# Performance work log

Hardware: AMD Instinct MI355X
Metric: run time of the kernel (lower is better)

## Reference

```python
import jax, jax.numpy as jnp
import numpy as np

B, T, N, D, R, K, P = 4, 336, 862, 64, 8, 6, 96


def setup_inputs() -> dict:
    key = jax.random.key(0)
    ks = jax.random.split(key, 8)
    s = 0.02
    return {
        "x_enc": jax.random.normal(ks[0], (B, T, N), jnp.float32),
        "W_embed": jax.random.normal(ks[1], (1, D), jnp.float32) * s,
        "b_embed": jnp.zeros((D,), jnp.float32),
        "W1": jax.random.normal(ks[2], (D, R), jnp.float32) * s,
        "W2": jax.random.normal(ks[3], (D, R), jnp.float32) * s,
        "gate": jnp.float32(-4.0),  # gate_init
        "A_prior": jnp.eye(N, dtype=jnp.float32),  # season_gcn_adj_source=identity
        "W_gcn": jax.random.normal(ks[4], (D, D), jnp.float32) * s,
        "g_gcn": jnp.float32(0.5),  # season_gcn gate
        "W_head": jax.random.normal(ks[5], (T * D, P), jnp.float32) * s,
        "b_head": jnp.zeros((P,), jnp.float32),
    }


def _topk_renorm(adj, k):
    # keep top-k entries per row, zero the rest, renormalize rows (matches _sparsify_adj)
    vals = jax.lax.top_k(adj, k)[0]
    thresh = vals[..., -1:]
    mask = (adj >= thresh).astype(adj.dtype)
    masked = adj * mask
    denom = jnp.clip(jnp.sum(masked, axis=-1, keepdims=True), 1e-12, None)
    return masked / denom


def reference(x_enc, W_embed, b_embed, W1, W2, gate, A_prior, W_gcn, g_gcn, W_head, b_head):
    # per-variable, per-timestep value embedding: [B,N,T,D]
    h = x_enc.transpose(0, 2, 1)[..., None] * W_embed[0] + b_embed
    # content-mean node descriptors: [B,N,D]
    z = jnp.mean(h, axis=2)
    # low-rank graph learner -> adjacency logits [B,N,N]
    e1 = z @ W1
    e2 = z @ W2
    logits = jnp.einsum('bnr,bmr->bnm', e1, e2) / jnp.sqrt(jnp.float32(R))
    adj = jax.nn.softmax(logits, axis=-1)
    adj = _topk_renorm(adj, K)  # top-k sparsify + row renorm
    # gated graph mixing over variable nodes
    h_mix = jnp.einsum('bnm,bmtd->bntd', adj, h)
    h = h + jax.nn.sigmoid(gate) * h_mix
    # season GCN: sym-normalized prior adjacency, residual + gate
    deg = jnp.sum(A_prior, axis=-1)
    dinv = jnp.where(deg > 0, 1.0 / jnp.sqrt(deg), 0.0)
    A_hat = A_prior * dinv[:, None] * dinv[None, :]
    h = h + g_gcn * jnp.einsum('nm,bmtd,de->bnte', A_hat, h, W_gcn)
    # forecast head: flatten tokens, project to pred_len per variable
    out = h.reshape(B, N, T * D) @ W_head + b_head  # [B,N,P]
    return out.transpose(0, 2, 1)  # [B,P,N]
```

## Files before the change

### kernel.cpp

```cpp
#include <hip/hip_runtime.h>
#include <math.h>

#define B_ 4
#define T_ 336
#define N_ 862
#define D_ 64
#define R_ 8
#define K_ 6
#define P_ 96
#define NR 896
#define CAP 32
#define NB 864

#define OFF_PCQ  0
#define OFF_XBP  768
#define OFF_DINV 21504
#define OFF_WGT  22368
#define OFF_IDX  43104
#define OFF_CNT  63840
#define OFF_CSRV 64704
#define OFF_CSRI 92352
#define OFF_P12  120000
#define OFF_PCP  184512
#define OFF_XPT  249024

__global__ __launch_bounds__(192) void kA_prep(const float* __restrict__ x,
                                               const float* __restrict__ Whead,
                                               const float* __restrict__ A,
                                               const float* __restrict__ We,
                                               const float* __restrict__ be,
                                               const float* __restrict__ gate,
                                               const float* __restrict__ Wgcn,
                                               float* __restrict__ ws) {
  int id = blockIdx.x;
  int tid = threadIdx.x;
  if (id < 336) {
    __shared__ float sW1[64], sW2[64], sCB[64], sWe[64];
    int t = id;
    float g = 1.f / (1.f + expf(-gate[0]));
    if (tid < 64) {
      float a = 0.f;
#pragma unroll
      for (int dd = 0; dd < D_; ++dd) a += We[dd] * Wgcn[dd * D_ + tid];
      sW1[tid] = a;
    } else if (tid < 128) {
      int e = tid - 64;
      float a = 0.f;
#pragma unroll
      for (int dd = 0; dd < D_; ++dd) a += be[dd] * Wgcn[dd * D_ + e];
      sW2[e] = (1.f + g) * a;
    } else {
      int e = tid - 128;
      sCB[e] = (1.f + g) * be[e];
      sWe[e] = We[e];
    }
    __syncthreads();
    int c = tid, p = c % P_, sel = c / P_;
    const float* cA = sel ? sW1 : sWe;
    const float* cB = sel ? sW2 : sCB;
    const float* wrow = Whead + (size_t)t * D_ * P_ + p;
    float a = 0.f, bacc = 0.f;
#pragma unroll
    for (int e = 0; e < D_; ++e) {
      float w = wrow[(size_t)e * P_];
      a = fmaf(cA[e], w, a);
      bacc = fmaf(cB[e], w, bacc);
    }
    ws[OFF_P12 + t * 192 + c] = a;
    ws[OFF_PCP + t * 192 + c] = bacc;
  } else if (id < 672) {
    __shared__ float part[192];
    int iq = id - 336;
    int b = iq / 84, rem = iq % 84;
    int ch = rem / 6, tg = rem % 6;
    int lane = tid & 63, tsub = tid >> 6;
    int n = ch * 64 + lane;
    float s = 0.f;
    if (n < N_) {
      const float* xp = x + (size_t)(b * T_) * N_ + n;
      int tend = tg * 56 + 56;
#pragma unroll 4
      for (int t = tg * 56 + tsub; t < tend; t += 3) s += xp[(size_t)t * N_];
    }
    part[tid] = s;
    __syncthreads();
    if (tsub == 0 && n < N_)
      ws[OFF_XBP + (size_t)(b * 6 + tg) * NB + n] =
          part[lane] + part[64 + lane] + part[128 + lane];
  } else {
    int lane = tid & 63, wv = tid >> 6;
    int n = (id - 672) * 3 + wv;
    if (n >= N_) return;
    const float* ap = A + (size_t)n * N_;
    float* vout = ws + OFF_CSRV;
    int* iout = (int*)(ws + OFF_CSRI);
    float s = 0.f;
    int total = 0;
    for (int base = 0; base < N_; base += 64) {
      int m = base + lane;
      float a = (m < N_) ? ap[m] : 0.f;
      s += a;
      bool nz = (a != 0.f);
      unsigned long long mask = __ballot(nz);
      int pos = __popcll(mask & ((1ull << lane) - 1ull));
      if (nz) {
        int slot = total + pos;
        if (slot < CAP) { vout[slot * NB + n] = a; iout[slot * NB + n] = m; }
      }
      total += __popcll(mask);
    }
    for (int off = 32; off; off >>= 1) s += __shfl_down(s, off);
    if (lane == 0) {
      ws[OFF_DINV + n] = (s > 0.f) ? (1.f / sqrtf(s)) : 0.f;
      ((int*)(ws + OFF_CNT))[n] = (total <= CAP) ? total : -1;
    }
  }
}

__global__ __launch_bounds__(192) void kM_mid(const float* __restrict__ x,
                                              const float* __restrict__ W1,
                                              const float* __restrict__ W2,
                                              const float* __restrict__ We,
                                              const float* __restrict__ be,
                                              const float* __restrict__ gate,
                                              float* __restrict__ ws) {
  __shared__ float smem[5376];
  int id = blockIdx.x;
  int tid = threadIdx.x;
  if (id < 432) {
    float* xs = smem;
    float* ps = smem + 768;
    int b = id / 108;
    int rem = id % 108;
    int n0 = (rem >> 1) * 16;
    int ch = (rem & 1) * 96;
    int cq = tid % 24, nq = tid / 24;
    int c0 = cq * 4;
    const float* P = ws + OFF_P12;
    float acc[4][2];
#pragma unroll
    for (int i = 0; i < 4; ++i) { acc[i][0] = 0.f; acc[i][1] = 0.f; }
    int xrow = tid >> 2, xcol4 = tid & 3;
    for (int kc = 0; kc < 7; ++kc) {
      int t0 = kc * 48;
      {
        const float* xr = x + (size_t)(b * T_ + t0 + xrow) * N_;
        if (n0 + 15 < N_) {
          *(float4*)(xs + xrow * 16 + xcol4 * 4) = *(const float4*)(xr + n0 + xcol4 * 4);
        } else {
          float* dst = xs + xrow * 16 + xcol4 * 4;
#pragma unroll
          for (int q = 0; q < 4; ++q) {
            int nn = n0 + xcol4 * 4 + q; if (nn > N_ - 1) nn = N_ - 1;
            dst[q] = xr[nn];
          }
        }
      }
#pragma unroll
      for (int sIdx = 0; sIdx < 6; ++sIdx) {
        int i4 = tid + sIdx * 192;
        int row = i4 / 24, col4 = i4 % 24;
        *(float4*)(ps + row * 96 + col4 * 4) =
            *(const float4*)(P + (size_t)(t0 + row) * 192 + ch + col4 * 4);
      }
      __syncthreads();
#pragma unroll 6
      for (int kk = 0; kk < 48; ++kk) {
        float x0 = xs[kk * 16 + nq * 2];
        float x1 = xs[kk * 16 + nq * 2 + 1];
        float4 pv = *(const float4*)(ps + kk * 96 + c0);
        acc[0][0] = fmaf(pv.x, x0, acc[0][0]); acc[0][1] = fmaf(pv.x, x1, acc[0][1]);
        acc[1][0] = fmaf(pv.y, x0, acc[1][0]); acc[1][1] = fmaf(pv.y, x1, acc[1][1]);
        acc[2][0] = fmaf(pv.z, x0, acc[2][0]); acc[2][1] = fmaf(pv.z, x1, acc[2][1]);
        acc[3][0] = fmaf(pv.w, x0, acc[3][0]); acc[3][1] = fmaf(pv.w, x1, acc[3][1]);
      }
      __syncthreads();
    }
    int n = n0 + nq * 2;
#pragma unroll
    for (int cc = 0; cc < 4; ++cc) {
      float* op = ws + OFF_XPT + ((size_t)(b * 192 + ch + c0 + cc)) * NR + n;
      if (n + 1 < N_) { float2 v; v.x = acc[cc][0]; v.y = acc[cc][1]; *(float2*)op = v; }
      else if (n < N_) { op[0] = acc[cc][0]; }
    }
  } else if (id < 436) {
    __shared__ float s_sc[4][R_];
    __shared__ float s_scal[5];
    __shared__ float selv[12];
    __shared__ int seli[12];
    float* sx = smem;
    float* wkmax = smem + 864;
    float* wkmin = smem + 1728;
    int b = id - 432;
    if (tid < 16) {
      int r = tid & 7, which = tid >> 3;
      const float* W = which ? W2 : W1;
      float a = 0.f, bb = 0.f;
      for (int dd = 0; dd < D_; ++dd) {
        float w = W[dd * R_ + r];
        a += We[dd] * w; bb += be[dd] * w;
      }
      s_sc[which * 2][r] = a; s_sc[which * 2 + 1][r] = bb;
    }
    const float invT = 1.f / (float)T_;
    for (int i = tid; i < NB; i += 192) {
      float v = 0.f;
      if (i < N_) {
        const float* xp = ws + OFF_XBP + (size_t)(b * 6) * NB + i;
#pragma unroll
        for (int q = 0; q < 6; ++q) v += xp[q * NB];
        v *= invT;
      }
      sx[i] = v;
      wkmax[i] = (i < N_) ? v : -3.4e38f;
      wkmin[i] = (i < N_) ? v : 3.4e38f;
    }
    __syncthreads();
    if (tid == 0) {
      float s11 = 0.f, s12 = 0.f, s21 = 0.f, s22 = 0.f;
      for (int r = 0; r < R_; ++r) {
        s11 += s_sc[0][r] * s_sc[2][r];
        s12 += s_sc[0][r] * s_sc[3][r];
        s21 += s_sc[1][r] * s_sc[2][r];
        s22 += s_sc[1][r] * s_sc[3][r];
      }
      s_scal[0] = s11; s_scal[1] = s12; s_scal[2] = s21; s_scal[3] = s22;
      s_scal[4] = 1.f / (1.f + expf(-gate[0]));
    }
    if (tid < 64) {
      int lane = tid;
      for (int r = 0; r < K_; ++r) {
        float bv = -3.4e38f; int bi = 0;
        for (int i = lane; i < N_; i += 64) {
          float v = wkmax[i];
          if (v > bv) { bv = v; bi = i; }
        }
        for (int off = 32; off; off >>= 1) {
          float ov = __shfl_down(bv, off);
          int oi = __shfl_down(bi, off);
          if (ov > bv) { bv = ov; bi = oi; }
        }
        bv = __shfl(bv, 0); bi = __shfl(bi, 0);
        if (lane == 0) { selv[r] = bv; seli[r] = bi; wkmax[bi] = -3.4e38f; }
      }
    } else if (tid < 128) {
      int lane = tid - 64;
      for (int r = 0; r < K_; ++r) {
        float bv = 3.4e38f; int bi = 0;
        for (int i = lane; i < N_; i += 64) {
          float v = wkmin[i];
          if (v < bv) { bv = v; bi = i; }
        }
        for (int off = 32; off; off >>= 1) {
          float ov = __shfl_down(bv, off);
          int oi = __shfl_down(bi, off);
          if (ov < bv) { bv = ov; bi = oi; }
        }
        bv = __shfl(bv, 0); bi = __shfl(bi, 0);
        if (lane == 0) { selv[6 + r] = bv; seli[6 + r] = bi; wkmin[bi] = 3.4e38f; }
      }
    }
    __syncthreads();
    float s11 = s_scal[0], s12 = s_scal[1], s21 = s_scal[2], s22 = s_scal[3];
    float g = s_scal[4];
    const float rsq = 0.3535533906f;
    for (int n = tid; n < N_; n += 192) {
      float xn = sx[n];
      float alpha = (xn * s11 + s21) * rsq;
      float beta  = (xn * s12 + s22) * rsq;
      int base = (alpha >= 0.f) ? 0 : 6;
      float l[K_]; float mx = -3.4e38f;
#pragma unroll
      for (int j = 0; j < K_; ++j) { l[j] = alpha * selv[base + j] + beta; mx = fmaxf(mx, l[j]); }
      float e[K_]; float ss = 0.f;
#pragma unroll
      for (int j = 0; j < K_; ++j) { e[j] = expf(l[j] - mx); ss += e[j]; }
      float sc = g / ss;
#pragma unroll
      for (int j = 0; j < K_; ++j) {
        ws[OFF_WGT + j * (4 * NB) + b * NB + n] = e[j] * sc;
        ((int*)(ws + OFF_IDX))[j * (4 * NB) + b * NB + n] = seli[base + j];
      }
    }
  } else {
    int q = id - 436;
    if (tid < 192) {
      float s = 0.f;
#pragma unroll 12
      for (int t = q * 84; t < q * 84 + 84; ++t) s += ws[OFF_PCP + t * 192 + tid];
      ws[OFF_PCQ + q * 192 + tid] = s;
    }
  }
}

__global__ __launch_bounds__(256) void kF_final(const float* __restrict__ A,
                                                const float* __restrict__ bhead,
                                                const float* __restrict__ ggcn,
                                                const float* __restrict__ ws,
                                                float* __restrict__ out) {
  int c = blockIdx.y;
  int n = blockIdx.x * 256 + threadIdx.x;
  if (n >= N_) return;
  int b = c / P_, p = c % P_;
  const float* Xp1 = ws + OFF_XPT + ((size_t)(b * 192 + p)) * NR;
  const float* Xp2 = ws + OFF_XPT + ((size_t)(b * 192 + P_ + p)) * NR;
  const float* WGTb = ws + OFF_WGT + b * NB;
  const int* IDXb = (const int*)(ws + OFF_IDX) + b * NB;
  float gg = ggcn[0];
  float PCp = 0.f, PAp = 0.f;
#pragma unroll
  for (int q = 0; q < 4; ++q) {
    PCp += ws[OFF_PCQ + q * 192 + p];
    PAp += ws[OFF_PCQ + q * 192 + 96 + p];
  }
  float wj[K_]; int ij[K_];
#pragma unroll
  for (int j = 0; j < K_; ++j) {
    wj[j] = WGTb[j * (4 * NB) + n];
    ij[j] = IDXb[j * (4 * NB) + n];
  }
  float acc1 = Xp1[n];
#pragma unroll
  for (int j = 0; j < K_; ++j) acc1 += wj[j] * Xp1[ij[j]];
  int cnt = ((const int*)(ws + OFF_CNT))[n];
  float S = 0.f;
  if (cnt >= 0) {
    const float* vv = ws + OFF_CSRV;
    const int* ii = (const int*)(ws + OFF_CSRI);
    for (int jj = 0; jj < cnt; ++jj) {
      float a = vv[jj * NB + n];
      int m = ii[jj * NB + n];
      float mix2 = Xp2[m];
      if (m == n) {
#pragma unroll
        for (int j = 0; j < K_; ++j) mix2 += wj[j] * Xp2[ij[j]];
      } else {
#pragma unroll
        for (int j = 0; j < K_; ++j)
          mix2 += WGTb[j * (4 * NB) + m] * Xp2[IDXb[j * (4 * NB) + m]];
      }
      S += a * ws[OFF_DINV + m] * (mix2 + PAp);
    }
  } else {
    const float* ar = A + (size_t)n * N_;
    for (int m = 0; m < N_; ++m) {
      float a = ar[m];
      if (a != 0.f) {
        float mix2 = Xp2[m];
#pragma unroll
        for (int j = 0; j < K_; ++j)
          mix2 += WGTb[j * (4 * NB) + m] * Xp2[IDXb[j * (4 * NB) + m]];
        S += a * ws[OFF_DINV + m] * (mix2 + PAp);
      }
    }
  }
  out[(size_t)c * N_ + n] = acc1 + gg * ws[OFF_DINV + n] * S + PCp + bhead[p];
}

extern "C" void kernel_launch(void* const* d_in, const int* in_sizes, int n_in,
                              void* d_out, int out_size, void* d_ws, size_t ws_size,
                              hipStream_t stream) {
  const float* x     = (const float*)d_in[0];
  const float* We    = (const float*)d_in[1];
  const float* be    = (const float*)d_in[2];
  const float* W1    = (const float*)d_in[3];
  const float* W2    = (const float*)d_in[4];
  const float* gate  = (const float*)d_in[5];
  const float* A     = (const float*)d_in[6];
  const float* Wgcn  = (const float*)d_in[7];
  const float* ggcn  = (const float*)d_in[8];
  const float* Whead = (const float*)d_in[9];
  const float* bhead = (const float*)d_in[10];
  float* ws = (float*)d_ws;
  float* out = (float*)d_out;

  kA_prep<<<960, 192, 0, stream>>>(x, Whead, A, We, be, gate, Wgcn, ws);
  kM_mid<<<440, 192, 0, stream>>>(x, W1, W2, We, be, gate, ws);
  kF_final<<<dim3(4, 384), 256, 0, stream>>>(A, bhead, ggcn, ws, out);
}
```

Baseline: 110.2 us.

## Fuse three kernels into one persistent kernel with atomic grid barriers

Merges the prep, mid and final kernels into a single persistent kernel of 512 blocks that loops over virtual block indices and separates the stages with software grid barriers built on atomic counters. A memset before the launch clears the barrier counters. The goal is to remove the launch gaps and tail drain between kernels. In exchange it adds barrier spin costs, leaves threads idle in stages written for 192 threads, adds a memset call, and relies on all 512 blocks being co-resident to avoid deadlock.

```diff
diff --git a/kernel.cpp b/kernel.cpp
--- a/kernel.cpp
+++ b/kernel.cpp
@@ -23,338 +23,360 @@
 #define OFF_P12  120000
 #define OFF_PCP  184512
 #define OFF_XPT  249024
-
-__global__ __launch_bounds__(192) void kA_prep(const float* __restrict__ x,
-                                               const float* __restrict__ Whead,
-                                               const float* __restrict__ A,
-                                               const float* __restrict__ We,
-                                               const float* __restrict__ be,
-                                               const float* __restrict__ gate,
-                                               const float* __restrict__ Wgcn,
-                                               float* __restrict__ ws) {
-  int id = blockIdx.x;
+#define OFF_BAR  937216
+
+#define GRID_ 512
+
+__device__ __forceinline__ void grid_barrier(int* ctr) {
+  __threadfence();
+  __syncthreads();
+  if (threadIdx.x == 0) {
+    __hip_atomic_fetch_add(ctr, 1, __ATOMIC_ACQ_REL, __HIP_MEMORY_SCOPE_AGENT);
+    while (__hip_atomic_load(ctr, __ATOMIC_ACQUIRE, __HIP_MEMORY_SCOPE_AGENT) < GRID_) {
+      __builtin_amdgcn_s_sleep(2);
+    }
+  }
+  __syncthreads();
+  __threadfence();
+}
+
+__global__ __launch_bounds__(256, 2) void kFused(
+    const float* __restrict__ x,    const float* __restrict__ We,
+    const float* __restrict__ be,   const float* __restrict__ W1,
+    const float* __restrict__ W2,   const float* __restrict__ gate,
+    const float* __restrict__ A,    const float* __restrict__ Wgcn,
+    const float* __restrict__ ggcn, const float* __restrict__ Whead,
+    const float* __restrict__ bhead, float* __restrict__ ws,
+    float* __restrict__ out) {
+  __shared__ float smem[5376];
   int tid = threadIdx.x;
-  if (id < 336) {
-    __shared__ float sW1[64], sW2[64], sCB[64], sWe[64];
-    int t = id;
-    float g = 1.f / (1.f + expf(-gate[0]));
-    if (tid < 64) {
-      float a = 0.f;
-#pragma unroll
-      for (int dd = 0; dd < D_; ++dd) a += We[dd] * Wgcn[dd * D_ + tid];
-      sW1[tid] = a;
-    } else if (tid < 128) {
-      int e = tid - 64;
-      float a = 0.f;
-#pragma unroll
-      for (int dd = 0; dd < D_; ++dd) a += be[dd] * Wgcn[dd * D_ + e];
-      sW2[e] = (1.f + g) * a;
+
+  for (int vb = blockIdx.x; vb < 888; vb += GRID_) {
+    __syncthreads();
+    if (vb < 336) {
+      float* sW1 = smem;
+      float* sW2 = smem + 64;
+      float* sCB = smem + 128;
+      float* sWe = smem + 192;
+      int t = vb;
+      float g = 1.f / (1.f + expf(-gate[0]));
+      if (tid < 64) {
+        float a = 0.f;
+#pragma unroll
+        for (int dd = 0; dd < D_; ++dd) a += We[dd] * Wgcn[dd * D_ + tid];
+        sW1[tid] = a;
+      } else if (tid < 128) {
+        int e = tid - 64;
+        float a = 0.f;
+#pragma unroll
+        for (int dd = 0; dd < D_; ++dd) a += be[dd] * Wgcn[dd * D_ + e];
+        sW2[e] = (1.f + g) * a;
+      } else if (tid < 192) {
+        int e = tid - 128;
+        sCB[e] = (1.f + g) * be[e];
+        sWe[e] = We[e];
+      }
+      __syncthreads();
+      if (tid < 192) {
+        int c = tid, p = c % P_, sel = c / P_;
+        const float* cA = sel ? sW1 : sWe;
+        const float* cB = sel ? sW2 : sCB;
+        const float* wrow = Whead + (size_t)t * D_ * P_ + p;
+        float a = 0.f, bacc = 0.f;
+#pragma unroll
+        for (int e = 0; e < D_; ++e) {
+          float w = wrow[(size_t)e * P_];
+          a = fmaf(cA[e], w, a);
+          bacc = fmaf(cB[e], w, bacc);
+        }
+        ws[OFF_P12 + t * 192 + c] = a;
+        ws[OFF_PCP + t * 192 + c] = bacc;
+      }
+    } else if (vb < 672) {
+      float* part = smem;
+      int iq = vb - 336;
+      int b = iq / 84, rem = iq % 84;
+      int ch = rem / 6, tg = rem % 6;
+      int lane = tid & 63, tsub = tid >> 6;
+      int n = ch * 64 + lane;
+      float s = 0.f;
+      if (n < N_) {
+        const float* xp = x + (size_t)(b * T_) * N_ + n;
+        int tend = tg * 56 + 56;
+#pragma unroll 4
+        for (int t = tg * 56 + tsub; t < tend; t += 4) s += xp[(size_t)t * N_];
+      }
+      part[tid] = s;
+      __syncthreads();
+      if (tsub == 0 && n < N_)
+        ws[OFF_XBP + (size_t)(b * 6 + tg) * NB + n] =
+            part[lane] + part[64 + lane] + part[128 + lane] + part[192 + lane];
     } else {
-      int e = tid - 128;
-      sCB[e] = (1.f + g) * be[e];
-      sWe[e] = We[e];
-    }
+      int lane = tid & 63, wv = tid >> 6;
+      int n = (vb - 672) * 4 + wv;
+      if (n < N_) {
+        const float* ap = A + (size_t)n * N_;
+        float* vout = ws + OFF_CSRV;
+        int* iout = (int*)(ws + OFF_CSRI);
+        float s = 0.f;
+        int total = 0;
+        for (int base = 0; base < N_; base += 64) {
+          int m = base + lane;
+          float a = (m < N_) ? ap[m] : 0.f;
+          s += a;
+          bool nz = (a != 0.f);
+          unsigned long long mask = __ballot(nz);
+          int pos = __popcll(mask & ((1ull << lane) - 1ull));
+          if (nz) {
+            int slot = total + pos;
+            if (slot < CAP) { vout[slot * NB + n] = a; iout[slot * NB + n] = m; }
+          }
+          total += __popcll(mask);
+        }
+        for (int off = 32; off; off >>= 1) s += __shfl_down(s, off);
+        if (lane == 0) {
+          ws[OFF_DINV + n] = (s > 0.f) ? (1.f / sqrtf(s)) : 0.f;
+          ((int*)(ws + OFF_CNT))[n] = (total <= CAP) ? total : -1;
+        }
+      }
+    }
+  }
+
+  grid_barrier((int*)(ws + OFF_BAR));
+
+  for (int vb = blockIdx.x; vb < 440; vb += GRID_) {
     __syncthreads();
-    int c = tid, p = c % P_, sel = c / P_;
-    const float* cA = sel ? sW1 : sWe;
-    const float* cB = sel ? sW2 : sCB;
-    const float* wrow = Whead + (size_t)t * D_ * P_ + p;
-    float a = 0.f, bacc = 0.f;
-#pragma unroll
-    for (int e = 0; e < D_; ++e) {
-      float w = wrow[(size_t)e * P_];
-      a = fmaf(cA[e], w, a);
-      bacc = fmaf(cB[e], w, bacc);
-    }
-    ws[OFF_P12 + t * 192 + c] = a;
-    ws[OFF_PCP + t * 192 + c] = bacc;
-  } else if (id < 672) {
-    __shared__ float part[192];
-    int iq = id - 336;
-    int b = iq / 84, rem = iq % 84;
-    int ch = rem / 6, tg = rem % 6;
-    int lane = tid & 63, tsub = tid >> 6;
-    int n = ch * 64 + lane;
-    float s = 0.f;
-    if (n < N_) {
-      const float* xp = x + (size_t)(b * T_) * N_ + n;
-      int tend = tg * 56 + 56;
-#pragma unroll 4
-      for (int t = tg * 56 + tsub; t < tend; t += 3) s += xp[(size_t)t * N_];
-    }
-    part[tid] = s;
-    __syncthreads();
-    if (tsub == 0 && n < N_)
-      ws[OFF_XBP + (size_t)(b * 6 + tg) * NB + n] =
-          part[lane] + part[64 + lane] + part[128 + lane];
-  } else {
-    int lane = tid & 63, wv = tid >> 6;
-    int n = (id - 672) * 3 + wv;
-    if (n >= N_) return;
-    const float* ap = A + (size_t)n * N_;
-    float* vout = ws + OFF_CSRV;
-    int* iout = (int*)(ws + OFF_CSRI);
-    float s = 0.f;
-    int total = 0;
-    for (int base = 0; base < N_; base += 64) {
-      int m = base + lane;
-      float a = (m < N_) ? ap[m] : 0.f;
-      s += a;
-      bool nz = (a != 0.f);
-      unsigned long long mask = __ballot(nz);
-      int pos = __popcll(mask & ((1ull << lane) - 1ull));
-      if (nz) {
-        int slot = total + pos;
-        if (slot < CAP) { vout[slot * NB + n] = a; iout[slot * NB + n] = m; }
-      }
-      total += __popcll(mask);
-    }
-    for (int off = 32; off; off >>= 1) s += __shfl_down(s, off);
-    if (lane == 0) {
-      ws[OFF_DINV + n] = (s > 0.f) ? (1.f / sqrtf(s)) : 0.f;
-      ((int*)(ws + OFF_CNT))[n] = (total <= CAP) ? total : -1;
+    if (vb < 432) {
+      float* xs = smem;
+      float* ps = smem + 768;
+      int b = vb / 108;
+      int rem = vb % 108;
+      int n0 = (rem >> 1) * 16;
+      int ch = (rem & 1) * 96;
+      int cq = tid % 24, nq = tid / 24;
+      int c0 = cq * 4;
+      const float* Pm = ws + OFF_P12;
+      float acc[4][2];
+#pragma unroll
+      for (int i = 0; i < 4; ++i) { acc[i][0] = 0.f; acc[i][1] = 0.f; }
+      int xrow = tid >> 2, xcol4 = tid & 3;
+      for (int kc = 0; kc < 7; ++kc) {
+        int t0 = kc * 48;
+        if (tid < 192) {
+          const float* xr = x + (size_t)(b * T_ + t0 + xrow) * N_;
+          if (n0 + 15 < N_) {
+            *(float4*)(xs + xrow * 16 + xcol4 * 4) = *(const float4*)(xr + n0 + xcol4 * 4);
+          } else {
+            float* dst = xs + xrow * 16 + xcol4 * 4;
+#pragma unroll
+            for (int q = 0; q < 4; ++q) {
+              int nn = n0 + xcol4 * 4 + q; if (nn > N_ - 1) nn = N_ - 1;
+              dst[q] = xr[nn];
+            }
+          }
+#pragma unroll
+          for (int sIdx = 0; sIdx < 6; ++sIdx) {
+            int i4 = tid + sIdx * 192;
+            int row = i4 / 24, col4 = i4 % 24;
+            *(float4*)(ps + row * 96 + col4 * 4) =
+                *(const float4*)(Pm + (size_t)(t0 + row) * 192 + ch + col4 * 4);
+          }
+        }
+        __syncthreads();
+        if (tid < 192) {
+#pragma unroll 6
+          for (int kk = 0; kk < 48; ++kk) {
+            float x0 = xs[kk * 16 + nq * 2];
+            float x1 = xs[kk * 16 + nq * 2 + 1];
+            float4 pv = *(const float4*)(ps + kk * 96 + c0);
+            acc[0][0] = fmaf(pv.x, x0, acc[0][0]); acc[0][1] = fmaf(pv.x, x1, acc[0][1]);
+            acc[1][0] = fmaf(pv.y, x0, acc[1][0]); acc[1][1] = fmaf(pv.y, x1, acc[1][1]);
+            acc[2][0] = fmaf(pv.z, x0, acc[2][0]); acc[2][1] = fmaf(pv.z, x1, acc[2][1]);
+            acc[3][0] = fmaf(pv.w, x0, acc[3][0]); acc[3][1] = fmaf(pv.w, x1, acc[3][1]);
+          }
+        }
+        __syncthreads();
+      }
+      if (tid < 192) {
+        int n = n0 + nq * 2;
+#pragma unroll
+        for (int cc = 0; cc < 4; ++cc) {
+          float* op = ws + OFF_XPT + ((size_t)(b * 192 + ch + c0 + cc)) * NR + n;
+          if (n + 1 < N_) { float2 v; v.x = acc[cc][0]; v.y = acc[cc][1]; *(float2*)op = v; }
+          else if (n < N_) { op[0] = acc[cc][0]; }
+        }
+      }
+    } else if (vb < 436) {
+      float* sx    = smem;
+      float* wkmax = smem + 864;
+      float* wkmin = smem + 1728;
+      float* s_sc  = smem + 2592;
+      float* s_scal = smem + 2624;
+      float* selv  = smem + 2629;
+      int*   seli  = (int*)(smem + 2641);
+      int b = vb - 432;
+      if (tid < 16) {
+        int r = tid & 7, which = tid >> 3;
+        const float* W = which ? W2 : W1;
+        float a = 0.f, bb = 0.f;
+        for (int dd = 0; dd < D_; ++dd) {
+          float w = W[dd * R_ + r];
+          a += We[dd] * w; bb += be[dd] * w;
+        }
+        s_sc[(which * 2) * 8 + r] = a; s_sc[(which * 2 + 1) * 8 + r] = bb;
+      }
+      const float invT = 1.f / (float)T_;
+      for (int i = tid; i < NB; i += 256) {
+        float v = 0.f;
+        if (i < N_) {
+          const float* xp = ws + OFF_XBP + (size_t)(b * 6) * NB + i;
+#pragma unroll
+          for (int q = 0; q < 6; ++q) v += xp[q * NB];
+          v *= invT;
+        }
+        sx[i] = v;
+        wkmax[i] = (i < N_) ? v : -3.4e38f;
+        wkmin[i] = (i < N_) ? v : 3.4e38f;
+      }
+      __syncthreads();
+      if (tid == 0) {
+        float s11 = 0.f, s12 = 0.f, s21 = 0.f, s22 = 0.f;
+        for (int r = 0; r < R_; ++r) {
+          s11 += s_sc[0 * 8 + r] * s_sc[2 * 8 + r];
+          s12 += s_sc[0 * 8 + r] * s_sc[3 * 8 + r];
+          s21 += s_sc[1 * 8 + r] * s_sc[2 * 8 + r];
+          s22 += s_sc[1 * 8 + r] * s_sc[3 * 8 + r];
+        }
+        s_scal[0] = s11; s_scal[1] = s12; s_scal[2] = s21; s_scal[3] = s22;
+        s_scal[4] = 1.f / (1.f + expf(-gate[0]));
+      }
+      if (tid < 64) {
+        int lane = tid;
+        for (int r = 0; r < K_; ++r) {
+          float bv = -3.4e38f; int bi = 0;
+          for (int i = lane; i < N_; i += 64) {
+            float v = wkmax[i];
+            if (v > bv) { bv = v; bi = i; }
+          }
+          for (int off = 32; off; off >>= 1) {
+            float ov = __shfl_down(bv, off);
+            int oi = __shfl_down(bi, off);
+            if (ov > bv) { bv = ov; bi = oi; }
+          }
+          bv = __shfl(bv, 0); bi = __shfl(bi, 0);
+          if (lane == 0) { selv[r] = bv; seli[r] = bi; wkmax[bi] = -3.4e38f; }
+        }
+      } else if (tid < 128) {
+        int lane = tid - 64;
+        for (int r = 0; r < K_; ++r) {
+          float bv = 3.4e38f; int bi = 0;
+          for (int i = lane; i < N_; i += 64) {
+            float v = wkmin[i];
+            if (v < bv) { bv = v; bi = i; }
+          }
+          for (int off = 32; off; off >>= 1) {
+            float ov = __shfl_down(bv, off);
+            int oi = __shfl_down(bi, off);
+            if (ov < bv) { bv = ov; bi = oi; }
+          }
+          bv = __shfl(bv, 0); bi = __shfl(bi, 0);
+          if (lane == 0) { selv[6 + r] = bv; seli[6 + r] = bi; wkmin[bi] = 3.4e38f; }
+        }
+      }
+      __syncthreads();
+      float s11 = s_scal[0], s12 = s_scal[1], s21 = s_scal[2], s22 = s_scal[3];
+      float g = s_scal[4];
+      const float rsq = 0.3535533906f;
+      for (int n = tid; n < N_; n += 256) {
+        float xn = sx[n];
+        float alpha = (xn * s11 + s21) * rsq;
+        float beta  = (xn * s12 + s22) * rsq;
+        int base = (alpha >= 0.f) ? 0 : 6;
+        float l[K_]; float mx = -3.4e38f;
+#pragma unroll
+        for (int j = 0; j < K_; ++j) { l[j] = alpha * selv[base + j] + beta; mx = fmaxf(mx, l[j]); }
+        float e[K_]; float ss = 0.f;
+#pragma unroll
+        for (int j = 0; j < K_; ++j) { e[j] = expf(l[j] - mx); ss += e[j]; }
+        float sc = g / ss;
+#pragma unroll
+        for (int j = 0; j < K_; ++j) {
+          ws[OFF_WGT + j * (4 * NB) + b * NB + n] = e[j] * sc;
+          ((int*)(ws + OFF_IDX))[j * (4 * NB) + b * NB + n] = seli[base + j];
+        }
+      }
+    } else {
+      int q = vb - 436;
+      if (tid < 192) {
+        float s = 0.f;
+#pragma unroll 12
+        for (int t = q * 84; t < q * 84 + 84; ++t) s += ws[OFF_PCP + t * 192 + tid];
+        ws[OFF_PCQ + q * 192 + tid] = s;
+      }
     }
   }
-}
-
-__global__ __launch_bounds__(192) void kM_mid(const float* __restrict__ x,
-                                              const float* __restrict__ W1,
-                                              const float* __restrict__ W2,
-                                              const float* __restrict__ We,
-                                              const float* __restrict__ be,
-                                              const float* __restrict__ gate,
-                                              float* __restrict__ ws) {
-  __shared__ float smem[5376];
-  int id = blockIdx.x;
-  int tid = threadIdx.x;
-  if (id < 432) {
-    float* xs = smem;
-    float* ps = smem + 768;
-    int b = id / 108;
-    int rem = id % 108;
-    int n0 = (rem >> 1) * 16;
-    int ch = (rem & 1) * 96;
-    int cq = tid % 24, nq = tid / 24;
-    int c0 = cq * 4;
-    const float* P = ws + OFF_P12;
-    float acc[4][2];
-#pragma unroll
-    for (int i = 0; i < 4; ++i) { acc[i][0] = 0.f; acc[i][1] = 0.f; }
-    int xrow = tid >> 2, xcol4 = tid & 3;
-    for (int kc = 0; kc < 7; ++kc) {
-      int t0 = kc * 48;
-      {
-        const float* xr = x + (size_t)(b * T_ + t0 + xrow) * N_;
-        if (n0 + 15 < N_) {
-          *(float4*)(xs + xrow * 16 + xcol4 * 4) = *(const float4*)(xr + n0 + xcol4 * 4);
+
+  grid_barrier((int*)(ws + OFF_BAR) + 8);
+
+  for (int vb = blockIdx.x; vb < 1536; vb += GRID_) {
+    int c = vb >> 2;
+    int n = (vb & 3) * 256 + tid;
+    if (n >= N_) continue;
+    int b = c / P_, p = c % P_;
+    const float* Xp1 = ws + OFF_XPT + ((size_t)(b * 192 + p)) * NR;
+    const float* Xp2 = ws + OFF_XPT + ((size_t)(b * 192 + P_ + p)) * NR;
+    const float* WGTb = ws + OFF_WGT + b * NB;
+    const int* IDXb = (const int*)(ws + OFF_IDX) + b * NB;
+    float gg = ggcn[0];
+    float PCp = 0.f, PAp = 0.f;
+#pragma unroll
+    for (int q = 0; q < 4; ++q) {
+      PCp += ws[OFF_PCQ + q * 192 + p];
+      PAp += ws[OFF_PCQ + q * 192 + 96 + p];
+    }
+    float wj[K_]; int ij[K_];
+#pragma unroll
+    for (int j = 0; j < K_; ++j) {
+      wj[j] = WGTb[j * (4 * NB) + n];
+      ij[j] = IDXb[j * (4 * NB) + n];
+    }
+    float acc1 = Xp1[n];
+#pragma unroll
+    for (int j = 0; j < K_; ++j) acc1 += wj[j] * Xp1[ij[j]];
+    int cnt = ((const int*)(ws + OFF_CNT))[n];
+    float S = 0.f;
+    if (cnt >= 0) {
+      const float* vv = ws + OFF_CSRV;
+      const int* ii = (const int*)(ws + OFF_CSRI);
+      for (int jj = 0; jj < cnt; ++jj) {
+        float a = vv[jj * NB + n];
+        int m = ii[jj * NB + n];
+        float mix2 = Xp2[m];
+        if (m == n) {
+#pragma unroll
+          for (int j = 0; j < K_; ++j) mix2 += wj[j] * Xp2[ij[j]];
         } else {
-          float* dst = xs + xrow * 16 + xcol4 * 4;
-#pragma unroll
-          for (int q = 0; q < 4; ++q) {
-            int nn = n0 + xcol4 * 4 + q; if (nn > N_ - 1) nn = N_ - 1;
-            dst[q] = xr[nn];
-          }
-        }
-      }
-#pragma unroll
-      for (int sIdx = 0; sIdx < 6; ++sIdx) {
-        int i4 = tid + sIdx * 192;
-        int row = i4 / 24, col4 = i4 % 24;
-        *(float4*)(ps + row * 96 + col4 * 4) =
-            *(const float4*)(P + (size_t)(t0 + row) * 192 + ch + col4 * 4);
-      }
-      __syncthreads();
-#pragma unroll 6
-      for (int kk = 0; kk < 48; ++kk) {
-        float x0 = xs[kk * 16 + nq * 2];
-        float x1 = xs[kk * 16 + nq * 2 + 1];
-        float4 pv = *(const float4*)(ps + kk * 96 + c0);
-        acc[0][0] = fmaf(pv.x, x0, acc[0][0]); acc[0][1] = fmaf(pv.x, x1, acc[0][1]);
-        acc[1][0] = fmaf(pv.y, x0, acc[1][0]); acc[1][1] = fmaf(pv.y, x1, acc[1][1]);
-        acc[2][0] = fmaf(pv.z, x0, acc[2][0]); acc[2][1] = fmaf(pv.z, x1, acc[2][1]);
-        acc[3][0] = fmaf(pv.w, x0, acc[3][0]); acc[3][1] = fmaf(pv.w, x1, acc[3][1]);
-      }
-      __syncthreads();
-    }
-    int n = n0 + nq * 2;
-#pragma unroll
-    for (int cc = 0; cc < 4; ++cc) {
-      float* op = ws + OFF_XPT + ((size_t)(b * 192 + ch + c0 + cc)) * NR + n;
-      if (n + 1 < N_) { float2 v; v.x = acc[cc][0]; v.y = acc[cc][1]; *(float2*)op = v; }
-      else if (n < N_) { op[0] = acc[cc][0]; }
-    }
-  } else if (id < 436) {
-    __shared__ float s_sc[4][R_];
-    __shared__ float s_scal[5];
-    __shared__ float selv[12];
-    __shared__ int seli[12];
-    float* sx = smem;
-    float* wkmax = smem + 864;
-    float* wkmin = smem + 1728;
-    int b = id - 432;
-    if (tid < 16) {
-      int r = tid & 7, which = tid >> 3;
-      const float* W = which ? W2 : W1;
-      float a = 0.f, bb = 0.f;
-      for (int dd = 0; dd < D_; ++dd) {
-        float w = W[dd * R_ + r];
-        a += We[dd] * w; bb += be[dd] * w;
-      }
-      s_sc[which * 2][r] = a; s_sc[which * 2 + 1][r] = bb;
-    }
-    const float invT = 1.f / (float)T_;
-    for (int i = tid; i < NB; i += 192) {
-      float v = 0.f;
-      if (i < N_) {
-        const float* xp = ws + OFF_XBP + (size_t)(b * 6) * NB + i;
-#pragma unroll
-        for (int q = 0; q < 6; ++q) v += xp[q * NB];
-        v *= invT;
-      }
-      sx[i] = v;
-      wkmax[i] = (i < N_) ? v : -3.4e38f;
-      wkmin[i] = (i < N_) ? v : 3.4e38f;
-    }
-    __syncthreads();
-    if (tid == 0) {
-      float s11 = 0.f, s12 = 0.f, s21 = 0.f, s22 = 0.f;
-      for (int r = 0; r < R_; ++r) {
-        s11 += s_sc[0][r] * s_sc[2][r];
-        s12 += s_sc[0][r] * s_sc[3][r];
-        s21 += s_sc[1][r] * s_sc[2][r];
-        s22 += s_sc[1][r] * s_sc[3][r];
-      }
-      s_scal[0] = s11; s_scal[1] = s12; s_scal[2] = s21; s_scal[3] = s22;
-      s_scal[4] = 1.f / (1.f + expf(-gate[0]));
-    }
-    if (tid < 64) {
-      int lane = tid;
-      for (int r = 0; r < K_; ++r) {
-        float bv = -3.4e38f; int bi = 0;
-        for (int i = lane; i < N_; i += 64) {
-          float v = wkmax[i];
-          if (v > bv) { bv = v; bi = i; }
-        }
-        for (int off = 32; off; off >>= 1) {
-          float ov = __shfl_down(bv, off);
-          int oi = __shfl_down(bi, off);
-          if (ov > bv) { bv = ov; bi = oi; }
-        }
-        bv = __shfl(bv, 0); bi = __shfl(bi, 0);
-        if (lane == 0) { selv[r] = bv; seli[r] = bi; wkmax[bi] = -3.4e38f; }
-      }
-    } else if (tid < 128) {
-      int lane = tid - 64;
-      for (int r = 0; r < K_; ++r) {
-        float bv = 3.4e38f; int bi = 0;
-        for (int i = lane; i < N_; i += 64) {
-          float v = wkmin[i];
-          if (v < bv) { bv = v; bi = i; }
-        }
-        for (int off = 32; off; off >>= 1) {
-          float ov = __shfl_down(bv, off);
-          int oi = __shfl_down(bi, off);
-          if (ov < bv) { bv = ov; bi = oi; }
-        }
-        bv = __shfl(bv, 0); bi = __shfl(bi, 0);
-        if (lane == 0) { selv[6 + r] = bv; seli[6 + r] = bi; wkmin[bi] = 3.4e38f; }
-      }
-    }
-    __syncthreads();
-    float s11 = s_scal[0], s12 = s_scal[1], s21 = s_scal[2], s22 = s_scal[3];
-    float g = s_scal[4];
-    const float rsq = 0.3535533906f;
-    for (int n = tid; n < N_; n += 192) {
-      float xn = sx[n];
-      float alpha = (xn * s11 + s21) * rsq;
-      float beta  = (xn * s12 + s22) * rsq;
-      int base = (alpha >= 0.f) ? 0 : 6;
-      float l[K_]; float mx = -3.4e38f;
-#pragma unroll
-      for (int j = 0; j < K_; ++j) { l[j] = alpha * selv[base + j] + beta; mx = fmaxf(mx, l[j]); }
-      float e[K_]; float ss = 0.f;
-#pragma unroll
-      for (int j = 0; j < K_; ++j) { e[j] = expf(l[j] - mx); ss += e[j]; }
-      float sc = g / ss;
-#pragma unroll
-      for (int j = 0; j < K_; ++j) {
-        ws[OFF_WGT + j * (4 * NB) + b * NB + n] = e[j] * sc;
-        ((int*)(ws + OFF_IDX))[j * (4 * NB) + b * NB + n] = seli[base + j];
-      }
-    }
-  } else {
-    int q = id - 436;
-    if (tid < 192) {
-      float s = 0.f;
-#pragma unroll 12
-      for (int t = q * 84; t < q * 84 + 84; ++t) s += ws[OFF_PCP + t * 192 + tid];
-      ws[OFF_PCQ + q * 192 + tid] = s;
-    }
+#pragma unroll
+          for (int j = 0; j < K_; ++j)
+            mix2 += WGTb[j * (4 * NB) + m] * Xp2[IDXb[j * (4 * NB) + m]];
+        }
+        S += a * ws[OFF_DINV + m] * (mix2 + PAp);
+      }
+    } else {
+      const float* ar = A + (size_t)n * N_;
+      for (int m = 0; m < N_; ++m) {
+        float a = ar[m];
+        if (a != 0.f) {
+          float mix2 = Xp2[m];
+#pragma unroll
+          for (int j = 0; j < K_; ++j)
+            mix2 += WGTb[j * (4 * NB) + m] * Xp2[IDXb[j * (4 * NB) + m]];
+          S += a * ws[OFF_DINV + m] * (mix2 + PAp);
+        }
+      }
+    }
+    out[(size_t)c * N_ + n] = acc1 + gg * ws[OFF_DINV + n] * S + PCp + bhead[p];
   }
-}
-
-__global__ __launch_bounds__(256) void kF_final(const float* __restrict__ A,
-                                                const float* __restrict__ bhead,
-                                                const float* __restrict__ ggcn,
-                                                const float* __restrict__ ws,
-                                                float* __restrict__ out) {
-  int c = blockIdx.y;
-  int n = blockIdx.x * 256 + threadIdx.x;
-  if (n >= N_) return;
-  int b = c / P_, p = c % P_;
-  const float* Xp1 = ws + OFF_XPT + ((size_t)(b * 192 + p)) * NR;
-  const float* Xp2 = ws + OFF_XPT + ((size_t)(b * 192 + P_ + p)) * NR;
-  const float* WGTb = ws + OFF_WGT + b * NB;
-  const int* IDXb = (const int*)(ws + OFF_IDX) + b * NB;
-  float gg = ggcn[0];
-  float PCp = 0.f, PAp = 0.f;
-#pragma unroll
-  for (int q = 0; q < 4; ++q) {
-    PCp += ws[OFF_PCQ + q * 192 + p];
-    PAp += ws[OFF_PCQ + q * 192 + 96 + p];
-  }
-  float wj[K_]; int ij[K_];
-#pragma unroll
-  for (int j = 0; j < K_; ++j) {
-    wj[j] = WGTb[j * (4 * NB) + n];
-    ij[j] = IDXb[j * (4 * NB) + n];
-  }
-  float acc1 = Xp1[n];
-#pragma unroll
-  for (int j = 0; j < K_; ++j) acc1 += wj[j] * Xp1[ij[j]];
-  int cnt = ((const int*)(ws + OFF_CNT))[n];
-  float S = 0.f;
-  if (cnt >= 0) {
-    const float* vv = ws + OFF_CSRV;
-    const int* ii = (const int*)(ws + OFF_CSRI);
-    for (int jj = 0; jj < cnt; ++jj) {
-      float a = vv[jj * NB + n];
-      int m = ii[jj * NB + n];
-      float mix2 = Xp2[m];
-      if (m == n) {
-#pragma unroll
-        for (int j = 0; j < K_; ++j) mix2 += wj[j] * Xp2[ij[j]];
-      } else {
-#pragma unroll
-        for (int j = 0; j < K_; ++j)
-          mix2 += WGTb[j * (4 * NB) + m] * Xp2[IDXb[j * (4 * NB) + m]];
-      }
-      S += a * ws[OFF_DINV + m] * (mix2 + PAp);
-    }
-  } else {
-    const float* ar = A + (size_t)n * N_;
-    for (int m = 0; m < N_; ++m) {
-      float a = ar[m];
-      if (a != 0.f) {
-        float mix2 = Xp2[m];
-#pragma unroll
-        for (int j = 0; j < K_; ++j)
-          mix2 += WGTb[j * (4 * NB) + m] * Xp2[IDXb[j * (4 * NB) + m]];
-        S += a * ws[OFF_DINV + m] * (mix2 + PAp);
-      }
-    }
-  }
-  out[(size_t)c * N_ + n] = acc1 + gg * ws[OFF_DINV + n] * S + PCp + bhead[p];
 }
 
 extern "C" void kernel_launch(void* const* d_in, const int* in_sizes, int n_in,
@@ -374,7 +396,8 @@
   float* ws = (float*)d_ws;
   float* out = (float*)d_out;
 
-  kA_prep<<<960, 192, 0, stream>>>(x, Whead, A, We, be, gate, Wgcn, ws);
-  kM_mid<<<440, 192, 0, stream>>>(x, W1, W2, We, be, gate, ws);
-  kF_final<<<dim3(4, 384), 256, 0, stream>>>(A, bhead, ggcn, ws, out);
+  hipMemsetAsync(ws + OFF_BAR, 0, 64 * sizeof(float), stream);
+
+  kFused<<<GRID_, 256, 0, stream>>>(x, We, be, W1, W2, gate, A, Wgcn, ggcn,
+                                    Whead, bhead, ws, out);
 }
```

Measured after the change: 422.4 us. 283% more time.

## Double-buffer kM_mid shared tiles and pack top-k weights and indices per node

Applied to the files above, without the earlier changes.

The x/P shared-memory staging in kM_mid now uses two buffers, so the next chunk's global loads are issued before the current chunk is computed. The top-k weights and indices are also repacked from six planar arrays into one interleaved 16-float cell per node, which kF_final reads with three float4 loads instead of twelve scalar loads. The cost is double the shared memory per block, which may reduce occupancy, and a slightly larger workspace. Only one __syncthreads per iteration is visible around the buffer swap, so correctness depends on the barrier left at the end of the loop.

```diff
diff --git a/kernel.cpp b/kernel.cpp
--- a/kernel.cpp
+++ b/kernel.cpp
@@ -15,14 +15,13 @@
 #define OFF_PCQ  0
 #define OFF_XBP  768
 #define OFF_DINV 21504
-#define OFF_WGT  22368
-#define OFF_IDX  43104
-#define OFF_CNT  63840
-#define OFF_CSRV 64704
-#define OFF_CSRI 92352
-#define OFF_P12  120000
-#define OFF_PCP  184512
-#define OFF_XPT  249024
+#define OFF_WGI  22368
+#define OFF_CNT  77664
+#define OFF_CSRV 78528
+#define OFF_CSRI 106176
+#define OFF_P12  133824
+#define OFF_PCP  198336
+#define OFF_XPT  262848
 
 __global__ __launch_bounds__(192) void kA_prep(const float* __restrict__ x,
                                                const float* __restrict__ Whead,
@@ -124,12 +123,12 @@
                                               const float* __restrict__ be,
                                               const float* __restrict__ gate,
                                               float* __restrict__ ws) {
-  __shared__ float smem[5376];
+  __shared__ float smem[10752];
   int id = blockIdx.x;
   int tid = threadIdx.x;
   if (id < 432) {
     float* xs = smem;
-    float* ps = smem + 768;
+    float* ps = smem + 1536;
     int b = id / 108;
     int rem = id % 108;
     int n0 = (rem >> 1) * 16;
@@ -141,34 +140,43 @@
 #pragma unroll
     for (int i = 0; i < 4; ++i) { acc[i][0] = 0.f; acc[i][1] = 0.f; }
     int xrow = tid >> 2, xcol4 = tid & 3;
-    for (int kc = 0; kc < 7; ++kc) {
+
+    auto stage = [&](int kc, int buf) {
       int t0 = kc * 48;
-      {
-        const float* xr = x + (size_t)(b * T_ + t0 + xrow) * N_;
-        if (n0 + 15 < N_) {
-          *(float4*)(xs + xrow * 16 + xcol4 * 4) = *(const float4*)(xr + n0 + xcol4 * 4);
-        } else {
-          float* dst = xs + xrow * 16 + xcol4 * 4;
-#pragma unroll
-          for (int q = 0; q < 4; ++q) {
-            int nn = n0 + xcol4 * 4 + q; if (nn > N_ - 1) nn = N_ - 1;
-            dst[q] = xr[nn];
-          }
+      float* xd = xs + buf * 768;
+      float* pd = ps + buf * 4608;
+      const float* xr = x + (size_t)(b * T_ + t0 + xrow) * N_;
+      if (n0 + 15 < N_) {
+        *(float4*)(xd + xrow * 16 + xcol4 * 4) = *(const float4*)(xr + n0 + xcol4 * 4);
+      } else {
+        float* dst = xd + xrow * 16 + xcol4 * 4;
+#pragma unroll
+        for (int q = 0; q < 4; ++q) {
+          int nn = n0 + xcol4 * 4 + q; if (nn > N_ - 1) nn = N_ - 1;
+          dst[q] = xr[nn];
         }
       }
 #pragma unroll
       for (int sIdx = 0; sIdx < 6; ++sIdx) {
         int i4 = tid + sIdx * 192;
         int row = i4 / 24, col4 = i4 % 24;
-        *(float4*)(ps + row * 96 + col4 * 4) =
+        *(float4*)(pd + row * 96 + col4 * 4) =
             *(const float4*)(P + (size_t)(t0 + row) * 192 + ch + col4 * 4);
       }
-      __syncthreads();
+    };
+
+    stage(0, 0);
+    __syncthreads();
+    for (int kc = 0; kc < 7; ++kc) {
+      int cur = kc & 1;
+      if (kc < 6) stage(kc + 1, cur ^ 1);
+      const float* xsC = xs + cur * 768;
+      const float* psC = ps + cur * 4608;
 #pragma unroll 6
       for (int kk = 0; kk < 48; ++kk) {
-        float x0 = xs[kk * 16 + nq * 2];
-        float x1 = xs[kk * 16 + nq * 2 + 1];
-        float4 pv = *(const float4*)(ps + kk * 96 + c0);
+        float x0 = xsC[kk * 16 + nq * 2];
+        float x1 = xsC[kk * 16 + nq * 2 + 1];
+        float4 pv = *(const float4*)(psC + kk * 96 + c0);
         acc[0][0] = fmaf(pv.x, x0, acc[0][0]); acc[0][1] = fmaf(pv.x, x1, acc[0][1]);
         acc[1][0] = fmaf(pv.y, x0, acc[1][0]); acc[1][1] = fmaf(pv.y, x1, acc[1][1]);
         acc[2][0] = fmaf(pv.z, x0, acc[2][0]); acc[2][1] = fmaf(pv.z, x1, acc[2][1]);
@@ -276,11 +284,16 @@
 #pragma unroll
       for (int j = 0; j < K_; ++j) { e[j] = expf(l[j] - mx); ss += e[j]; }
       float sc = g / ss;
-#pragma unroll
-      for (int j = 0; j < K_; ++j) {
-        ws[OFF_WGT + j * (4 * NB) + b * NB + n] = e[j] * sc;
-        ((int*)(ws + OFF_IDX))[j * (4 * NB) + b * NB + n] = seli[base + j];
-      }
+      float4 v0, v1, v2;
+      v0.x = e[0] * sc; v0.y = e[1] * sc; v0.z = e[2] * sc; v0.w = e[3] * sc;
+      v1.x = e[4] * sc; v1.y = e[5] * sc;
+      v1.z = __int_as_float(seli[base + 0]); v1.w = __int_as_float(seli[base + 1]);
+      v2.x = __int_as_float(seli[base + 2]); v2.y = __int_as_float(seli[base + 3]);
+      v2.z = __int_as_float(seli[base + 4]); v2.w = __int_as_float(seli[base + 5]);
+      float* cell = ws + OFF_WGI + ((size_t)(b * NB + n)) * 16;
+      *(float4*)cell = v0;
+      *(float4*)(cell + 4) = v1;
+      *(float4*)(cell + 8) = v2;
     }
   } else {
     int q = id - 436;
@@ -304,8 +317,7 @@
   int b = c / P_, p = c % P_;
   const float* Xp1 = ws + OFF_XPT + ((size_t)(b * 192 + p)) * NR;
   const float* Xp2 = ws + OFF_XPT + ((size_t)(b * 192 + P_ + p)) * NR;
-  const float* WGTb = ws + OFF_WGT + b * NB;
-  const int* IDXb = (const int*)(ws + OFF_IDX) + b * NB;
+  const float* WGIb = ws + OFF_WGI + (size_t)b * NB * 16;
   float gg = ggcn[0];
   float PCp = 0.f, PAp = 0.f;
 #pragma unroll
@@ -313,12 +325,16 @@
     PCp += ws[OFF_PCQ + q * 192 + p];
     PAp += ws[OFF_PCQ + q * 192 + 96 + p];
   }
+  const float* cell = WGIb + (size_t)n * 16;
+  float4 u0 = *(const float4*)cell;
+  float4 u1 = *(const float4*)(cell + 4);
+  float4 u2 = *(const float4*)(cell + 8);
   float wj[K_]; int ij[K_];
-#pragma unroll
-  for (int j = 0; j < K_; ++j) {
-    wj[j] = WGTb[j * (4 * NB) + n];
-    ij[j] = IDXb[j * (4 * NB) + n];
-  }
+  wj[0] = u0.x; wj[1] = u0.y; wj[2] = u0.z; wj[3] = u0.w;
+  wj[4] = u1.x; wj[5] = u1.y;
+  ij[0] = __float_as_int(u1.z); ij[1] = __float_as_int(u1.w);
+  ij[2] = __float_as_int(u2.x); ij[3] = __float_as_int(u2.y);
+  ij[4] = __float_as_int(u2.z); ij[5] = __float_as_int(u2.w);
   float acc1 = Xp1[n];
 #pragma unroll
   for (int j = 0; j < K_; ++j) acc1 += wj[j] * Xp1[ij[j]];
@@ -335,9 +351,13 @@
 #pragma unroll
         for (int j = 0; j < K_; ++j) mix2 += wj[j] * Xp2[ij[j]];
       } else {
-#pragma unroll
-        for (int j = 0; j < K_; ++j)
-          mix2 += WGTb[j * (4 * NB) + m] * Xp2[IDXb[j * (4 * NB) + m]];
+        const float* mc = WGIb + (size_t)m * 16;
+        float4 a0 = *(const float4*)mc;
+        float4 a1 = *(const float4*)(mc + 4);
+        float4 a2 = *(const float4*)(mc + 8);
+        mix2 += a0.x * Xp2[__float_as_int(a1.z)] + a0.y * Xp2[__float_as_int(a1.w)]
+              + a0.z * Xp2[__float_as_int(a2.x)] + a0.w * Xp2[__float_as_int(a2.y)]
+              + a1.x * Xp2[__float_as_int(a2.z)] + a1.y * Xp2[__float_as_int(a2.w)];
       }
       S += a * ws[OFF_DINV + m] * (mix2 + PAp);
     }
@@ -346,10 +366,14 @@
     for (int m = 0; m < N_; ++m) {
       float a = ar[m];
       if (a != 0.f) {
-        float mix2 = Xp2[m];
-#pragma unroll
-        for (int j = 0; j < K_; ++j)
-          mix2 += WGTb[j * (4 * NB) + m] * Xp2[IDXb[j * (4 * NB) + m]];
+        const float* mc = WGIb + (size_t)m * 16;
+        float4 a0 = *(const float4*)mc;
+        float4 a1 = *(const float4*)(mc + 4);
+        float4 a2 = *(const float4*)(mc + 8);
+        float mix2 = Xp2[m]
+              + a0.x * Xp2[__float_as_int(a1.z)] + a0.y * Xp2[__float_as_int(a1.w)]
+              + a0.z * Xp2[__float_as_int(a2.x)] + a0.w * Xp2[__float_as_int(a2.y)]
+              + a1.x * Xp2[__float_as_int(a2.z)] + a1.y * Xp2[__float_as_int(a2.w)];
         S += a * ws[OFF_DINV + m] * (mix2 + PAp);
       }
     }
```

Result: no change. 109.2 us, median of 2 (-0.9%).
